# Performance work log

Hardware: AMD Instinct MI355X
Metric: run time of the kernel (lower is better)

Reference implementation:

```python
import jax, jax.numpy as jnp
import numpy as np

NUM_BINS = 256  # int(data_range + 1), data_range = 255.0
EPS = 1e-8


def setup_inputs() -> dict:
    key = jax.random.key(0)
    x = jax.random.uniform(key, (32, 3, 512, 512), dtype=jnp.float32)  # RGB in [0,1]
    return {"x": x}


def reference(x) -> jnp.ndarray:
    # to_y_channel(x, 255.0, 'yiq'): Y = 0.299R + 0.587G + 0.114B, scaled to [0,255], rounded
    y = (0.299 * x[:, 0] + 0.587 * x[:, 1] + 0.114 * x[:, 2]) * 255.0  # (N,H,W)
    vals = jnp.clip(jnp.round(y), 0, NUM_BINS - 1).astype(jnp.int32)
    n = x.shape[0]
    flat = vals.reshape(n, -1)  # (N, H*W)
    # per-image 256-bin histogram without materializing a one-hot tensor
    hist = jax.vmap(lambda v: jnp.bincount(v, length=NUM_BINS))(flat).astype(jnp.float32)
    hist = hist / jnp.sum(hist, axis=1, keepdims=True)
    score = -jnp.sum(hist * jnp.log2(hist + EPS), axis=1)  # (N,)
    return score
```

## Files before the change

### kernel.cpp

```cpp
#include <hip/hip_runtime.h>

#define NUM_BINS 256
#define HH 512
#define WW 512
#define PIX_PER_IMG (HH * WW)
#define CH_STRIDE (HH * WW)
#define IMG_STRIDE (3 * HH * WW)
#define BLOCKS_PER_IMG 64
#define THREADS 256

__global__ void zero_hist_kernel(unsigned int* __restrict__ hist) {
    hist[blockIdx.x * blockDim.x + threadIdx.x] = 0u;
}

__global__ __launch_bounds__(THREADS) void hist_kernel(const float* __restrict__ x,
                                                       unsigned int* __restrict__ g_hist) {
    __shared__ unsigned int sh[4][NUM_BINS];
    const int wave = threadIdx.x >> 6;

    for (int i = threadIdx.x; i < 4 * NUM_BINS; i += THREADS)
        ((unsigned int*)sh)[i] = 0u;
    __syncthreads();

    const int img = blockIdx.x / BLOCKS_PER_IMG;
    const int blk = blockIdx.x % BLOCKS_PER_IMG;

    const float* base = x + (size_t)img * IMG_STRIDE;
    const float4* r4 = (const float4*)(base);
    const float4* g4 = (const float4*)(base + CH_STRIDE);
    const float4* b4 = (const float4*)(base + 2 * CH_STRIDE);

    const int n4 = PIX_PER_IMG / 4;
    const int stride = BLOCKS_PER_IMG * THREADS;
    int tid = blk * THREADS + threadIdx.x;

    for (int i = tid; i < n4; i += stride) {
        float4 r = r4[i];
        float4 g = g4[i];
        float4 b = b4[i];

        float y0 = (0.299f * r.x + 0.587f * g.x + 0.114f * b.x) * 255.0f;
        float y1 = (0.299f * r.y + 0.587f * g.y + 0.114f * b.y) * 255.0f;
        float y2 = (0.299f * r.z + 0.587f * g.z + 0.114f * b.z) * 255.0f;
        float y3 = (0.299f * r.w + 0.587f * g.w + 0.114f * b.w) * 255.0f;

        int b0 = (int)rintf(y0);
        int b1 = (int)rintf(y1);
        int b2 = (int)rintf(y2);
        int b3 = (int)rintf(y3);
        b0 = min(max(b0, 0), NUM_BINS - 1);
        b1 = min(max(b1, 0), NUM_BINS - 1);
        b2 = min(max(b2, 0), NUM_BINS - 1);
        b3 = min(max(b3, 0), NUM_BINS - 1);

        atomicAdd(&sh[wave][b0], 1u);
        atomicAdd(&sh[wave][b1], 1u);
        atomicAdd(&sh[wave][b2], 1u);
        atomicAdd(&sh[wave][b3], 1u);
    }
    __syncthreads();

    for (int i = threadIdx.x; i < NUM_BINS; i += THREADS) {
        unsigned int s = sh[0][i] + sh[1][i] + sh[2][i] + sh[3][i];
        if (s) atomicAdd(&g_hist[img * NUM_BINS + i], s);
    }
}

__global__ __launch_bounds__(THREADS) void entropy_kernel(const unsigned int* __restrict__ g_hist,
                                                          float* __restrict__ out) {
    const int img = blockIdx.x;
    const int lane = threadIdx.x & 63;
    const int wave = threadIdx.x >> 6;

    unsigned int c = g_hist[img * NUM_BINS + threadIdx.x];
    float p = (float)c * (1.0f / (float)PIX_PER_IMG);
    float v = -p * log2f(p + 1e-8f);

    for (int o = 32; o > 0; o >>= 1)
        v += __shfl_down(v, o, 64);

    __shared__ float part[4];
    if (lane == 0) part[wave] = v;
    __syncthreads();
    if (threadIdx.x == 0)
        out[img] = part[0] + part[1] + part[2] + part[3];
}

extern "C" void kernel_launch(void* const* d_in, const int* in_sizes, int n_in,
                              void* d_out, int out_size, void* d_ws, size_t ws_size,
                              hipStream_t stream) {
    const float* x = (const float*)d_in[0];
    float* out = (float*)d_out;
    unsigned int* hist = (unsigned int*)d_ws;

    const int n_img = in_sizes[0] / IMG_STRIDE;

    zero_hist_kernel<<<n_img, NUM_BINS, 0, stream>>>(hist);
    hist_kernel<<<n_img * BLOCKS_PER_IMG, THREADS, 0, stream>>>(x, hist);
    entropy_kernel<<<n_img, THREADS, 0, stream>>>(hist, out);
}
```

Measured before the change: 144.1 us.

## Replace global histogram atomics with per-block partials reduced in entropy kernel

```diff
diff --git a/kernel.cpp b/kernel.cpp
--- a/kernel.cpp
+++ b/kernel.cpp
@@ -9,12 +9,8 @@
 #define BLOCKS_PER_IMG 64
 #define THREADS 256
 
-__global__ void zero_hist_kernel(unsigned int* __restrict__ hist) {
-    hist[blockIdx.x * blockDim.x + threadIdx.x] = 0u;
-}
-
 __global__ __launch_bounds__(THREADS) void hist_kernel(const float* __restrict__ x,
-                                                       unsigned int* __restrict__ g_hist) {
+                                                       unsigned int* __restrict__ part) {
     __shared__ unsigned int sh[4][NUM_BINS];
     const int wave = threadIdx.x >> 6;
 
@@ -60,30 +56,34 @@
     }
     __syncthreads();
 
-    for (int i = threadIdx.x; i < NUM_BINS; i += THREADS) {
-        unsigned int s = sh[0][i] + sh[1][i] + sh[2][i] + sh[3][i];
-        if (s) atomicAdd(&g_hist[img * NUM_BINS + i], s);
-    }
+    unsigned int* dst = part + (size_t)blockIdx.x * NUM_BINS;
+    for (int i = threadIdx.x; i < NUM_BINS; i += THREADS)
+        dst[i] = sh[0][i] + sh[1][i] + sh[2][i] + sh[3][i];
 }
 
-__global__ __launch_bounds__(THREADS) void entropy_kernel(const unsigned int* __restrict__ g_hist,
+__global__ __launch_bounds__(THREADS) void entropy_kernel(const unsigned int* __restrict__ part,
                                                           float* __restrict__ out) {
     const int img = blockIdx.x;
     const int lane = threadIdx.x & 63;
     const int wave = threadIdx.x >> 6;
 
-    unsigned int c = g_hist[img * NUM_BINS + threadIdx.x];
-    float p = (float)c * (1.0f / (float)PIX_PER_IMG);
-    float v = -p * log2f(p + 1e-8f);
+    const unsigned int* p = part + (size_t)img * BLOCKS_PER_IMG * NUM_BINS;
+    unsigned int c = 0;
+    #pragma unroll 8
+    for (int b = 0; b < BLOCKS_PER_IMG; ++b)
+        c += p[b * NUM_BINS + threadIdx.x];
+
+    float prob = (float)c * (1.0f / (float)PIX_PER_IMG);
+    float v = -prob * log2f(prob + 1e-8f);
 
     for (int o = 32; o > 0; o >>= 1)
         v += __shfl_down(v, o, 64);
 
-    __shared__ float part[4];
-    if (lane == 0) part[wave] = v;
+    __shared__ float pw[4];
+    if (lane == 0) pw[wave] = v;
     __syncthreads();
     if (threadIdx.x == 0)
-        out[img] = part[0] + part[1] + part[2] + part[3];
+        out[img] = pw[0] + pw[1] + pw[2] + pw[3];
 }
 
 extern "C" void kernel_launch(void* const* d_in, const int* in_sizes, int n_in,
@@ -91,11 +91,10 @@
                               hipStream_t stream) {
     const float* x = (const float*)d_in[0];
     float* out = (float*)d_out;
-    unsigned int* hist = (unsigned int*)d_ws;
+    unsigned int* part = (unsigned int*)d_ws;
 
     const int n_img = in_sizes[0] / IMG_STRIDE;
 
-    zero_hist_kernel<<<n_img, NUM_BINS, 0, stream>>>(hist);
-    hist_kernel<<<n_img * BLOCKS_PER_IMG, THREADS, 0, stream>>>(x, hist);
-    entropy_kernel<<<n_img, THREADS, 0, stream>>>(hist, out);
+    hist_kernel<<<n_img * BLOCKS_PER_IMG, THREADS, 0, stream>>>(x, part);
+    entropy_kernel<<<n_img, THREADS, 0, stream>>>(part, out);
 }
```

New measurement: 143.9 us. No clear change (-0.1%).
